# Kernel optimization log

Hardware: AMD Instinct MI355X
Metric: run time of the kernel (lower is better)

## Reference

```python
import jax, jax.numpy as jnp
import numpy as np

D = 200; H = 4; DH = D // H
N_ETYPE = 38; N_NTYPE = 4
B = 256; L = 1024; E = B * L
NODES_PER_G = 200; N = B * NODES_PER_G


def _bn(x, g, b):
    # BatchNorm1d in training mode: batch stats over rows (biased variance, eps=1e-5)
    m = x.mean(axis=0)
    v = x.var(axis=0)
    return (x - m) * jax.lax.rsqrt(v + 1e-5) * g + b


def setup_inputs():
    key = jax.random.key(0)
    ks = jax.random.split(key, 24)
    f = lambda k, s: jax.random.normal(k, s, jnp.float32) * 0.02
    head = jax.random.randint(ks[0], (E,), 0, N)
    tail = (head + 1 + jax.random.randint(ks[1], (E,), 0, N - 1)) % N  # guaranteed no self-loops
    return {
        "x": jax.random.normal(ks[2], (N, D), jnp.float32),
        "node_feature_extra": jax.random.normal(ks[3], (N, D), jnp.float32),
        "sent_vec_r": jax.random.normal(ks[4], (B, D), jnp.float32),
        "We1": f(ks[5], (N_ETYPE + 1 + 2 * N_NTYPE, D)), "be1": jnp.zeros((D,), jnp.float32),
        "ge1": jnp.ones((D,), jnp.float32), "bte1": jnp.zeros((D,), jnp.float32),
        "We2": f(ks[6], (D, D)), "be2": jnp.zeros((D,), jnp.float32),
        "Wa1": f(ks[7], (2 * D, D)), "ba1": jnp.zeros((D,), jnp.float32),
        "ga1": jnp.ones((D,), jnp.float32), "bta1": jnp.zeros((D,), jnp.float32),
        "Wa2": f(ks[8], (D, D)), "ba2": jnp.zeros((D,), jnp.float32),
        "Watt": f(ks[9], (D, D)),
        "Wk": f(ks[10], (2 * D, D)), "bk": jnp.zeros((D,), jnp.float32),
        "Wm": f(ks[11], (2 * D, D)), "bm": jnp.zeros((D,), jnp.float32),
        "Wq": f(ks[12], (D, D)), "bq": jnp.zeros((D,), jnp.float32),
        "Wo1": f(ks[13], (D, D)), "bo1": jnp.zeros((D,), jnp.float32),
        "go1": jnp.ones((D,), jnp.float32), "bto1": jnp.zeros((D,), jnp.float32),
        "Wo2": f(ks[14], (D, D)), "bo2": jnp.zeros((D,), jnp.float32),
        "edge_index": jnp.stack([head, tail]),
        "edge_type": jax.random.randint(ks[15], (E,), 0, N_ETYPE),
        "node_type": jax.random.randint(ks[16], (N,), 0, N_NTYPE),
        "edges_per_graph": L,
    }


def reference(x, node_feature_extra, sent_vec_r, We1, be1, ge1, bte1, We2, be2,
              Wa1, ba1, ga1, bta1, Wa2, ba2, Watt, Wk, bk, Wm, bm, Wq, bq,
              Wo1, bo1, go1, bto1, Wo2, bo2,
              edge_index, edge_type, node_type, edges_per_graph):
    E_, N_ = edge_index.shape[1], x.shape[0]
    src, dst = edge_index[0], edge_index[1]
    x_head, x_tail = x[src], x[dst]
    x_fact = x_tail - x_head
    nt = N_ETYPE + 1
    # original does this segment-mean on detached CPU numpy -> no gradient path
    xf = jax.lax.stop_gradient(x_fact)
    sums = jax.ops.segment_sum(xf, edge_type, num_segments=nt)
    cnts = jax.ops.segment_sum(jnp.ones((E_,), x.dtype), edge_type, num_segments=nt)
    result = (sums / jnp.maximum(cnts, 1.0)[:, None])[edge_type]  # [E, D]
    # one-hot edge/node-type features for real edges + self edges
    edge_vec = jax.nn.one_hot(edge_type, nt, dtype=x.dtype)
    self_edge_vec = jnp.zeros((N_, nt), x.dtype).at[:, N_ETYPE].set(1.0)
    ht = jnp.concatenate([jax.nn.one_hot(node_type[src], N_NTYPE, dtype=x.dtype),
                          jax.nn.one_hot(node_type[dst], N_NTYPE, dtype=x.dtype)], 1)
    sh = jax.nn.one_hot(node_type, N_NTYPE, dtype=x.dtype)
    feat = jnp.concatenate([jnp.concatenate([edge_vec, ht], 1),
                            jnp.concatenate([self_edge_vec, sh, sh], 1)], 0)  # [E+N, 47]
    emb = jax.nn.relu(_bn(feat @ We1 + be1, ge1, bte1)) @ We2 + be2  # edge_encoder, [E+N, D]
    emb_e, emb_self = emb[:E_], emb[E_:]
    # edge_encoder_again on cat([emb_e, result]); split matmul avoids the [E,2D] concat
    h2 = _bn(emb_e @ Wa1[:D] + result @ Wa1[D:] + ba1, ga1, bta1)
    R = jax.nn.relu(h2) @ Wa2 + ba2  # [E, D]
    # per-graph attention: Q rows within a graph are identical (repeated sent_vec),
    # so the LxL softmax has identical rows -> compute one row per graph and broadcast.
    Bg = E_ // edges_per_graph
    Rg = R.reshape(Bg, edges_per_graph, D)
    q = sent_vec_r @ Watt  # [B, D]
    scores = jnp.einsum('bd,bld->bl', q, Rg) / jnp.sqrt(jnp.asarray(D, x.dtype))
    attn = jax.nn.softmax(scores, axis=1)
    upd = jnp.einsum('bl,bld->bd', attn, Rg)
    updated_R = jnp.broadcast_to(upd[:, None, :], Rg.shape).reshape(E_, D)
    edge_attr = jnp.concatenate([updated_R, emb_self], 0)
    # append self-loops (input edge_index has none, matching remove_self_loops)
    loop = jnp.arange(N_, dtype=src.dtype)
    src_all = jnp.concatenate([src, loop])
    dst_all = jnp.concatenate([dst, loop])
    x_i, x_j = x[dst_all], x[src_all]
    key_ = (x_i @ Wk[:D] + edge_attr @ Wk[D:] + bk).reshape(-1, H, DH)
    msg = (x_j @ Wm[:D] + edge_attr @ Wm[D:] + bm).reshape(-1, H, DH)
    qry = ((x_j @ Wq + bq) / jnp.sqrt(jnp.asarray(DH, x.dtype))).reshape(-1, H, DH)
    sc = (qry * key_).sum(-1)  # [E+N, H]
    # segment softmax grouped by source node (every segment non-empty due to self-loops)
    smax = jax.ops.segment_max(sc, src_all, num_segments=N_)
    ex = jnp.exp(sc - smax[src_all])
    den = jax.ops.segment_sum(ex, src_all, num_segments=N_)
    alpha = ex / den[src_all]
    cnt = jax.ops.segment_sum(jnp.ones((src_all.shape[0],), x.dtype), src_all, num_segments=N_)
    alpha = alpha * cnt[src_all][:, None]
    m = (msg * alpha[:, :, None]).reshape(-1, D)
    aggr = jax.ops.segment_sum(m, dst_all, num_segments=N_)  # scatter-add at targets
    return jax.nn.relu(_bn(aggr @ Wo1 + bo1, go1, bto1)) @ Wo2 + bo2
```

## Files before the change

kernel.cpp:

```cpp
#include <hip/hip_runtime.h>

#define D     200
#define H     4
#define DH    50
#define NE    38
#define NTY   4
#define NC    608
#define NCT   612
#define BG    256
#define LG    1024
#define EE    262144
#define NN    51200
#define EA    313344
#define NB    200

#define NTILES 13
#define KSTEPS 7
#define NMATS  8
#define SLICE_SHORTS 13312
#define NCHUNK 26
#define MROWS  128

typedef __attribute__((ext_vector_type(4))) float  f32x4;
typedef __attribute__((ext_vector_type(8))) short  bf16x8;

__device__ __forceinline__ short bf_hi(float f) {
    unsigned u = __float_as_uint(f);
    unsigned r = u + 0x7fffu + ((u >> 16) & 1u);
    return (short)(r >> 16);
}
__device__ __forceinline__ float bf_f(short s) {
    return __uint_as_float(((unsigned)(unsigned short)s) << 16);
}

__global__ __launch_bounds__(256) void k_hist(const int* __restrict__ ei, const int* __restrict__ et,
                                              const int* __restrict__ nt, int* outdeg, int* indeg,
                                              int* __restrict__ hcnt, float* coef) {
    __shared__ int loc[NC];
    int g = blockIdx.x, t = threadIdx.x;
    for (int i = t; i < NC; i += 256) loc[i] = 0;
    __syncthreads();
    #pragma unroll
    for (int j = 0; j < 4; j++) {
        int e = g * LG + j * 256 + t;
        int s = ei[e], d = ei[EE + e], tp = et[e];
        int c = tp * 16 + nt[s] * 4 + nt[d];
        atomicAdd(&loc[c], 1);
        atomicAdd(&outdeg[s], 1);
        atomicAdd(&indeg[d], 1);
        unsafeAtomicAdd(&coef[(size_t)d * NE + tp],  1.f);
        unsafeAtomicAdd(&coef[(size_t)s * NE + tp], -1.f);
    }
    __syncthreads();
    for (int i = t; i < NC; i += 256) hcnt[g * NC + i] = loc[i];
}

__global__ __launch_bounds__(256) void k_hist2(const int* __restrict__ hcnt, int* __restrict__ hist) {
    int c = blockIdx.x * 256 + threadIdx.x;
    if (c >= NC) return;
    int s = 0;
    for (int g = 0; g < BG; g++) s += hcnt[g * NC + c];
    hist[c] = s;
}

__global__ __launch_bounds__(256) void k_ntcnt(const int* __restrict__ nt, int* ntcnt) {
    __shared__ int loc[NTY];
    int t = threadIdx.x;
    if (t < NTY) loc[t] = 0;
    __syncthreads();
    int n = blockIdx.x * 256 + t;
    if (n < NN) atomicAdd(&loc[nt[n]], 1);
    __syncthreads();
    if (t < NTY) atomicAdd(&ntcnt[t], loc[t]);
}

__global__ void k_tcnt(const int* __restrict__ hist, int* tcnt) {
    int t = threadIdx.x;
    if (t < NE) { int s = 0; for (int i = 0; i < 16; i++) s += hist[t*16 + i]; tcnt[t] = s; }
}

__global__ __launch_bounds__(256) void k_xfsum3(const float* __restrict__ x, const float* __restrict__ coef,
                                                float* sums) {
    const int CH = NN / 256;
    int t = threadIdx.x;
    int n0 = blockIdx.x * CH;
    float acc[NE];
    #pragma unroll
    for (int m = 0; m < NE; m++) acc[m] = 0.f;
    if (t < D) {
        for (int k = 0; k < CH; k++) {
            int n = n0 + k;
            float xv = x[(size_t)n * D + t];
            const float* cf = coef + (size_t)n * NE;
            #pragma unroll
            for (int m = 0; m < NE; m++) acc[m] += cf[m] * xv;
        }
        #pragma unroll
        for (int m = 0; m < NE; m++)
            if (acc[m] != 0.f) unsafeAtomicAdd(&sums[m * D + t], acc[m]);
    }
}

__global__ __launch_bounds__(256) void k_scan_a(const int* __restrict__ a, const int* __restrict__ b,
                                                int* bsA, int* bsB) {
    __shared__ int redA[4], redB[4];
    int t = threadIdx.x, blk = blockIdx.x;
    int i = blk * 256 + t;
    int va = a[i], vb = b[i];
    for (int o = 1; o < 64; o <<= 1) { va += __shfl_xor(va, o); vb += __shfl_xor(vb, o); }
    int wave = t >> 6, lane = t & 63;
    if (lane == 0) { redA[wave] = va; redB[wave] = vb; }
    __syncthreads();
    if (t == 0) {
        bsA[blk] = redA[0] + redA[1] + redA[2] + redA[3];
        bsB[blk] = redB[0] + redB[1] + redB[2] + redB[3];
    }
}

__global__ __launch_bounds__(256) void k_scan_b(int* bsA, int* bsB, int* aoff, int* boff) {
    __shared__ int pa[256], pb[256];
    int t = threadIdx.x;
    int va = (t < NB) ? bsA[t] : 0;
    int vb = (t < NB) ? bsB[t] : 0;
    pa[t] = va; pb[t] = vb;
    __syncthreads();
    for (int off = 1; off < 256; off <<= 1) {
        int xa = (t >= off) ? pa[t - off] : 0;
        int xb = (t >= off) ? pb[t - off] : 0;
        __syncthreads();
        pa[t] += xa; pb[t] += xb;
        __syncthreads();
    }
    if (t < NB) { bsA[t] = pa[t] - va; bsB[t] = pb[t] - vb; }
    if (t == NB - 1) { aoff[NN] = pa[t]; boff[NN] = pb[t]; }
}

__global__ __launch_bounds__(256) void k_scan_c(const int* __restrict__ a, const int* __restrict__ b,
                                                const int* __restrict__ bsA, const int* __restrict__ bsB,
                                                int* aoff, int* boff, int* acur, int* bcur) {
    __shared__ int wsA[4], wsB[4];
    int t = threadIdx.x, blk = blockIdx.x;
    int i = blk * 256 + t;
    int va = a[i], vb = b[i];
    int wave = t >> 6, lane = t & 63;
    int sa = va, sb = vb;
    for (int o = 1; o < 64; o <<= 1) {
        int xa = __shfl_up(sa, o);
        int xb = __shfl_up(sb, o);
        if (lane >= o) { sa += xa; sb += xb; }
    }
    if (lane == 63) { wsA[wave] = sa; wsB[wave] = sb; }
    __syncthreads();
    int baseA = bsA[blk], baseB = bsB[blk];
    #pragma unroll
    for (int wv = 0; wv < 3; wv++) {
        if (wv < wave) { baseA += wsA[wv]; baseB += wsB[wv]; }
    }
    int ea = baseA + sa - va;
    int eb = baseB + sb - vb;
    aoff[i] = ea; acur[i] = ea;
    boff[i] = eb; bcur[i] = eb;
}

__global__ __launch_bounds__(256) void k_scatter(const int* __restrict__ ei, int* scur, int* dcur,
                                                 int* slist, int* dlist) {
    int e = blockIdx.x * 256 + threadIdx.x;
    if (e >= EE) return;
    int s = ei[e], d = ei[EE + e];
    slist[atomicAdd(&scur[s], 1)] = e;
    dlist[atomicAdd(&dcur[d], 1)] = e;
}

__global__ __launch_bounds__(256) void k_combos1(const float* __restrict__ We1, const float* __restrict__ be1,
                                                 const int* __restrict__ hist, const int* __restrict__ ntcnt,
                                                 float* __restrict__ h1, float* bn1) {
    int c = blockIdx.x, d = threadIdx.x;
    if (d >= D) return;
    float v, w;
    if (c < NC) {
        int etp = c >> 4, ts = (c >> 2) & 3, td = c & 3;
        v = We1[etp*D + d] + We1[(39+ts)*D + d] + We1[(43+td)*D + d] + be1[d];
        w = (float)hist[c];
    } else {
        int t = c - NC;
        v = We1[38*D + d] + We1[(39+t)*D + d] + We1[(43+t)*D + d] + be1[d];
        w = (float)ntcnt[t];
    }
    h1[c*D + d] = v;
    unsafeAtomicAdd(&bn1[d], w * v);
    unsafeAtomicAdd(&bn1[D + d], w * v * v);
}

__global__ __launch_bounds__(256) void k_combos2(const float* __restrict__ h1, const float* __restrict__ bn1,
                                                 const float* __restrict__ ge1, const float* __restrict__ bte1,
                                                 const float* __restrict__ We2, const float* __restrict__ be2,
                                                 float* __restrict__ embE, float* __restrict__ embS) {
    __shared__ float v[D];
    int c = blockIdx.x, t = threadIdx.x;
    if (t < D) {
        float cnt = (float)(EE + NN);
        float m = bn1[t] / cnt;
        float var = bn1[D + t] / cnt - m * m;
        float r = rsqrtf(var + 1e-5f);
        float u = (h1[c*D + t] - m) * r * ge1[t] + bte1[t];
        v[t] = fmaxf(u, 0.f);
    }
    __syncthreads();
    if (t < D) {
        float acc = be2[t];
        for (int k = 0; k < D; k++) acc += v[k] * We2[k*D + t];
        if (c < NC) embE[c*D + t] = acc; else embS[(c-NC)*D + t] = acc;
    }
}

__global__ __launch_bounds__(256) void k_combos3(const float* __restrict__ embE, const float* __restrict__ sumsxf,
                                                 const int* __restrict__ tcnt, const float* __restrict__ Wa1,
                                                 const float* __restrict__ ba1, const int* __restrict__ hist,
                                                 float* __restrict__ h2, float* bn2) {
    __shared__ float a[2*D];
    int c = blockIdx.x, t = threadIdx.x;
    int etp = c >> 4;
    if (t < D) {
        a[t] = embE[c*D + t];
        float cn = fmaxf((float)tcnt[etp], 1.f);
        a[D + t] = sumsxf[etp*D + t] / cn;
    }
    __syncthreads();
    if (t < D) {
        float acc = ba1[t];
        for (int k = 0; k < 2*D; k++) acc += a[k] * Wa1[k*D + t];
        h2[c*D + t] = acc;
        float w = (float)hist[c];
        unsafeAtomicAdd(&bn2[t], w * acc);
        unsafeAtomicAdd(&bn2[D + t], w * acc * acc);
    }
}

__global__ __launch_bounds__(256) void k_combos4(const float* __restrict__ h2, const float* __restrict__ bn2,
                                                 const float* __restrict__ ga1, const float* __restrict__ bta1,
                                                 const float* __restrict__ Wa2, const float* __restrict__ ba2,
                                                 float* __restrict__ Rc, float* __restrict__ RcT) {
    __shared__ float v[D];
    int c = blockIdx.x, t = threadIdx.x;
    if (t < D) {
        float inv = 1.f / (float)EE;
        float m = bn2[t] * inv;
        float var = bn2[D + t] * inv - m * m;
        float r = rsqrtf(var + 1e-5f);
        float u = (h2[c*D + t] - m) * r * ga1[t] + bta1[t];
        v[t] = fmaxf(u, 0.f);
    }
    __syncthreads();
    if (t < D) {
        float acc = ba2[t];
        for (int k = 0; k < D; k++) acc += v[k] * Wa2[k*D + t];
        Rc[c*D + t] = acc;
        RcT[(size_t)t * NC + c] = acc;
    }
}

__global__ __launch_bounds__(512) void k_attn(const float* __restrict__ qs,
                                              const float* __restrict__ Rc, const float* __restrict__ RcT,
                                              const int* __restrict__ hcnt, float* __restrict__ upd) {
    __shared__ float q[D];
    __shared__ float w[NC];
    __shared__ float red[16];
    __shared__ float part[8][D];
    int b = blockIdx.x, t = threadIdx.x;
    int wave = t >> 6, lane = t & 63;
    if (t < D) q[t] = qs[b*D + t];
    __syncthreads();
    {
        float s0a = 0.f, s0b = 0.f, s0c = 0.f, s0d = 0.f;
        float s1a = 0.f, s1b = 0.f, s1c = 0.f, s1d = 0.f;
        for (int k = 0; k < D; k += 4) {
            float q0 = q[k], q1 = q[k+1], q2 = q[k+2], q3 = q[k+3];
            const float* r = RcT + (size_t)k * NC;
            s0a += q0 * r[t];
            s0b += q1 * r[NC + t];
            s0c += q2 * r[2*NC + t];
            s0d += q3 * r[3*NC + t];
            if (t < NC - 512) {
                s1a += q0 * r[t + 512];
                s1b += q1 * r[NC + t + 512];
                s1c += q2 * r[2*NC + t + 512];
                s1d += q3 * r[3*NC + t + 512];
            }
        }
        w[t] = (s0a + s0b) + (s0c + s0d);
        if (t < NC - 512) w[t + 512] = (s1a + s1b) + (s1c + s1d);
    }
    __syncthreads();
    float mx = -1e30f;
    for (int c = t; c < NC; c += 512) mx = fmaxf(mx, w[c]);
    for (int o = 32; o; o >>= 1) mx = fmaxf(mx, __shfl_xor(mx, o));
    if (lane == 0) red[wave] = mx;
    __syncthreads();
    mx = red[0];
    #pragma unroll
    for (int i = 1; i < 8; i++) mx = fmaxf(mx, red[i]);
    float sm = 0.f;
    for (int c = t; c < NC; c += 512) {
        float wv = (float)hcnt[b * NC + c] * __expf(w[c] - mx);
        w[c] = wv;
        sm += wv;
    }
    for (int o = 32; o; o >>= 1) sm += __shfl_xor(sm, o);
    if (lane == 0) red[8 + wave] = sm;
    __syncthreads();
    float tot = red[8];
    #pragma unroll
    for (int i = 1; i < 8; i++) tot += red[8 + i];
    float inv = 1.f / tot;
    float a4[4] = {0.f, 0.f, 0.f, 0.f};
    for (int c = wave * (NC/8); c < (wave + 1) * (NC/8); c++) {
        float wv = w[c];
        const float* r = Rc + c * D;
        #pragma unroll
        for (int j = 0; j < 4; j++) { int dd = lane + 64*j; if (dd < D) a4[j] += wv * r[dd]; }
    }
    #pragma unroll
    for (int j = 0; j < 4; j++) { int dd = lane + 64*j; if (dd < D) part[wave][dd] = a4[j]; }
    __syncthreads();
    if (t < D) {
        float s = part[0][t];
        #pragma unroll
        for (int i = 1; i < 8; i++) s += part[i][t];
        upd[b*D + t] = s * inv;
    }
}

__global__ __launch_bounds__(256) void k_packW(const float* __restrict__ Wk, const float* __restrict__ Wm,
                                               const float* __restrict__ Wq, const float* __restrict__ Wo1,
                                               const float* __restrict__ Wo2, const float* __restrict__ Watt,
                                               short* __restrict__ Bpk) {
    int blk = blockIdx.x;
    int mat = blk / (NTILES * KSTEPS);
    int rem = blk - mat * (NTILES * KSTEPS);
    int ks = rem / NTILES, nt = rem - ks * NTILES;
    const float* W = (mat == 0) ? Wk : (mat == 1) ? Wm : (mat == 2) ? Wq : (mat == 3) ? Wo1 :
                     (mat == 4) ? Wo2 : (mat == 5) ? Watt : (mat == 6) ? (Wk + D*D) : (Wm + D*D);
    int t = threadIdx.x;
    for (int idx = t; idx < 1024; idx += 256) {
        int split = idx >> 9;
        int lane = (idx & 511) >> 3;
        int j = idx & 7;
        int n = nt * 16 + (lane & 15);
        int k = ks * 32 + ((lane >> 4) << 3) + j;
        float v = (k < D && n < D) ? W[k * D + n] : 0.f;
        short h = bf_hi(v);
        short out = split ? bf_hi(v - bf_f(h)) : h;
        Bpk[(size_t)blk * 1024 + idx] = out;
    }
}

__device__ __forceinline__ void stage_load(const short* __restrict__ g, int w, int lane, f32x4 rg[7]) {
    #pragma unroll
    for (int i = 0; i < 7; i++) {
        int c = w + 4 * i;
        if (c < NCHUNK) rg[i] = *(const f32x4*)((const char*)g + c * 1024 + lane * 16);
    }
}
__device__ __forceinline__ void stage_write(short* l, int w, int lane, const f32x4 rg[7]) {
    #pragma unroll
    for (int i = 0; i < 7; i++) {
        int c = w + 4 * i;
        if (c < NCHUNK) *(f32x4*)((char*)l + c * 1024 + lane * 16) = rg[i];
    }
}

__device__ __forceinline__ void load_afrag(const float* __restrict__ A, int row, int quad, int ks,
                                           int preop, const float* __restrict__ bnacc, float invCnt,
                                           const float* __restrict__ g, const float* __restrict__ bb,
                                           bf16x8& ah, bf16x8& al) {
    int k0 = ks * 32 + quad * 8;
    float v[8];
    if (k0 < D) {
        const float* src = A + (size_t)row * D + k0;
        float4 p0 = *(const float4*)src;
        float4 p1 = *(const float4*)(src + 4);
        v[0]=p0.x; v[1]=p0.y; v[2]=p0.z; v[3]=p0.w;
        v[4]=p1.x; v[5]=p1.y; v[6]=p1.z; v[7]=p1.w;
        if (preop) {
            float4 m0 = *(const float4*)(bnacc + k0);
            float4 m1 = *(const float4*)(bnacc + k0 + 4);
            float4 q0 = *(const float4*)(bnacc + D + k0);
            float4 q1 = *(const float4*)(bnacc + D + k0 + 4);
            float4 g0 = *(const float4*)(g + k0);
            float4 g1 = *(const float4*)(g + k0 + 4);
            float4 b0 = *(const float4*)(bb + k0);
            float4 b1 = *(const float4*)(bb + k0 + 4);
            float mm[8] = {m0.x,m0.y,m0.z,m0.w,m1.x,m1.y,m1.z,m1.w};
            float qq[8] = {q0.x,q0.y,q0.z,q0.w,q1.x,q1.y,q1.z,q1.w};
            float gg[8] = {g0.x,g0.y,g0.z,g0.w,g1.x,g1.y,g1.z,g1.w};
            float bv[8] = {b0.x,b0.y,b0.z,b0.w,b1.x,b1.y,b1.z,b1.w};
            #pragma unroll
            for (int j = 0; j < 8; j++) {
                float mj = mm[j] * invCnt;
                float var = qq[j] * invCnt - mj * mj;
                float rs = rsqrtf(var + 1e-5f);
                float s = rs * gg[j];
                v[j] = fmaxf(v[j] * s + (bv[j] - mj * s), 0.f);
            }
        }
    } else {
        #pragma unroll
        for (int j = 0; j < 8; j++) v[j] = 0.f;
    }
    #pragma unroll
    for (int j = 0; j < 8; j++) {
        short h = bf_hi(v[j]);
        ah[j] = h;
        al[j] = bf_hi(v[j] - bf_f(h));
    }
}

__device__ __forceinline__ void store_C2(f32x4 acc0[NTILES], f32x4 acc1[NTILES], float* __restrict__ C,
                                         int n0, int w, int lane,
                                         const float* __restrict__ bias, float postscale) {
    int colb = lane & 15, quad = lane >> 4;
    int rbase = n0 + w * 32;
    #pragma unroll
    for (int nt = 0; nt < NTILES; nt++) {
        int col = nt * 16 + colb;
        if (col < D) {
            float bj = bias ? bias[col] : 0.f;
            #pragma unroll
            for (int r = 0; r < 4; r++) {
                int row = rbase + quad * 4 + r;
                C[(size_t)row * D + col]        = (acc0[nt][r] + bj) * postscale;
                C[(size_t)(row + 16) * D + col] = (acc1[nt][r] + bj) * postscale;
            }
        }
    }
}

#define MMF_KS(MATV, KS, NUTOT, BASE)                                           \
    {                                                                           \
        int u_ = (MATV) * KSTEPS + (KS);                                        \
        int cur_ = u_ & 1;                                                      \
        if (u_ + 1 < (NUTOT))                                                   \
            stage_load((BASE) + (size_t)(u_ + 1) * SLICE_SHORTS, w, lane, rg);  \
        bf16x8 ah0_, al0_, ah1_, al1_;                                          \
        load_afrag(A, row0, quad, KS, preop_, bnacc_, invCnt_, g_, bb_, ah0_, al0_); \
        load_afrag(A, row1, quad, KS, preop_, bnacc_, invCnt_, g_, bb_, ah1_, al1_); \
        const bf16x8* B8_ = (const bf16x8*)(Bls + cur_ * SLICE_SHORTS);         \
        _Pragma("unroll")                                                       \
        for (int nt = 0; nt < NTILES; nt++) {                                   \
            bf16x8 bh = B8_[nt * 128 + lane];                                   \
            bf16x8 bl = B8_[nt * 128 + 64 + lane];                              \
            acc0[nt] = __builtin_amdgcn_mfma_f32_16x16x32_bf16(al0_, bh, acc0[nt], 0, 0, 0); \
            acc0[nt] = __builtin_amdgcn_mfma_f32_16x16x32_bf16(ah0_, bl, acc0[nt], 0, 0, 0); \
            acc0[nt] = __builtin_amdgcn_mfma_f32_16x16x32_bf16(ah0_, bh, acc0[nt], 0, 0, 0); \
            acc1[nt] = __builtin_amdgcn_mfma_f32_16x16x32_bf16(al1_, bh, acc1[nt], 0, 0, 0); \
            acc1[nt] = __builtin_amdgcn_mfma_f32_16x16x32_bf16(ah1_, bl, acc1[nt], 0, 0, 0); \
            acc1[nt] = __builtin_amdgcn_mfma_f32_16x16x32_bf16(ah1_, bh, acc1[nt], 0, 0, 0); \
        }                                                                       \
        if (u_ + 1 < (NUTOT)) {                                                 \
            stage_write(Bls + (cur_ ^ 1) * SLICE_SHORTS, w, lane, rg);          \
            __syncthreads();                                                    \
        }                                                                       \
    }

__global__ __launch_bounds__(256, 2) void k_mmf3(const float* __restrict__ A, const short* __restrict__ Bpk,
                                                 const float* __restrict__ bq,
                                                 float* __restrict__ XK, float* __restrict__ XM, float* __restrict__ XQ) {
    __shared__ __align__(16) short Bls[2 * SLICE_SHORTS];
    int t = threadIdx.x, w = t >> 6, lane = t & 63;
    int n0 = blockIdx.x * MROWS;
    int row0 = n0 + w * 32 + (lane & 15);
    int row1 = row0 + 16;
    int quad = lane >> 4;
    int preop_ = 0; const float* bnacc_ = nullptr; float invCnt_ = 0.f;
    const float* g_ = nullptr; const float* bb_ = nullptr;
    f32x4 rg[7];
    stage_load(Bpk, w, lane, rg);
    stage_write(Bls, w, lane, rg);
    __syncthreads();
    f32x4 acc0[NTILES], acc1[NTILES];
    for (int mat = 0; mat < 3; ++mat) {
        #pragma unroll
        for (int nt = 0; nt < NTILES; nt++) {
            acc0[nt][0]=0.f; acc0[nt][1]=0.f; acc0[nt][2]=0.f; acc0[nt][3]=0.f;
            acc1[nt][0]=0.f; acc1[nt][1]=0.f; acc1[nt][2]=0.f; acc1[nt][3]=0.f;
        }
        MMF_KS(mat, 0, 3*KSTEPS, Bpk)
        MMF_KS(mat, 1, 3*KSTEPS, Bpk)
        MMF_KS(mat, 2, 3*KSTEPS, Bpk)
        MMF_KS(mat, 3, 3*KSTEPS, Bpk)
        MMF_KS(mat, 4, 3*KSTEPS, Bpk)
        MMF_KS(mat, 5, 3*KSTEPS, Bpk)
        MMF_KS(mat, 6, 3*KSTEPS, Bpk)
        if (mat == 0)      store_C2(acc0, acc1, XK, n0, w, lane, nullptr, 1.f);
        else if (mat == 1) store_C2(acc0, acc1, XM, n0, w, lane, nullptr, 1.f);
        else               store_C2(acc0, acc1, XQ, n0, w, lane, bq, 0.14142135623730950488f);
    }
}

__global__ __launch_bounds__(256, 2) void k_mmf(const float* __restrict__ A, const short* __restrict__ Bmat,
                                                const float* __restrict__ bias, float* __restrict__ C,
                                                int preop, const float* __restrict__ bnacc, float invCnt,
                                                const float* __restrict__ g, const float* __restrict__ bb,
                                                float postscale) {
    __shared__ __align__(16) short Bls[2 * SLICE_SHORTS];
    int t = threadIdx.x, w = t >> 6, lane = t & 63;
    int n0 = blockIdx.x * MROWS;
    int row0 = n0 + w * 32 + (lane & 15);
    int row1 = row0 + 16;
    int quad = lane >> 4;
    int preop_ = preop; const float* bnacc_ = bnacc; float invCnt_ = invCnt;
    const float* g_ = g; const float* bb_ = bb;
    f32x4 rg[7];
    stage_load(Bmat, w, lane, rg);
    stage_write(Bls, w, lane, rg);
    __syncthreads();
    f32x4 acc0[NTILES], acc1[NTILES];
    #pragma unroll
    for (int nt = 0; nt < NTILES; nt++) {
        acc0[nt][0]=0.f; acc0[nt][1]=0.f; acc0[nt][2]=0.f; acc0[nt][3]=0.f;
        acc1[nt][0]=0.f; acc1[nt][1]=0.f; acc1[nt][2]=0.f; acc1[nt][3]=0.f;
    }
    MMF_KS(0, 0, KSTEPS, Bmat)
    MMF_KS(0, 1, KSTEPS, Bmat)
    MMF_KS(0, 2, KSTEPS, Bmat)
    MMF_KS(0, 3, KSTEPS, Bmat)
    MMF_KS(0, 4, KSTEPS, Bmat)
    MMF_KS(0, 5, KSTEPS, Bmat)
    MMF_KS(0, 6, KSTEPS, Bmat)
    store_C2(acc0, acc1, C, n0, w, lane, bias, postscale);
}

__device__ __forceinline__ float head_reduce(float h0, float h1, float h2, float h3, int lane) {
    float ax = (lane < 32) ? h2 : h0;
    float ay = (lane < 32) ? h3 : h1;
    float u0 = ((lane < 32) ? h0 : h2) + __shfl_xor(ax, 32);
    float u1 = ((lane < 32) ? h1 : h3) + __shfl_xor(ay, 32);
    float bx = ((lane & 16) == 0) ? u1 : u0;
    float v  = (((lane & 16) == 0) ? u0 : u1) + __shfl_xor(bx, 16);
    v += __shfl_xor(v, 8);
    v += __shfl_xor(v, 4);
    v += __shfl_xor(v, 2);
    v += __shfl_xor(v, 1);
    return v;
}

__global__ __launch_bounds__(256) void k_soft(const int* __restrict__ ei, const int* __restrict__ nt,
                                              const int* __restrict__ soff, const int* __restrict__ slist,
                                              const int* __restrict__ outdeg,
                                              const float* __restrict__ XQ, const float* __restrict__ XK,
                                              const float* __restrict__ GK, const float* __restrict__ SK,
                                              float* __restrict__ sc, float* __restrict__ scale) {
    int wave = threadIdx.x >> 6, lane = threadIdx.x & 63;
    int n = blockIdx.x * 4 + wave;
    if (n >= NN) return;
    bool act = lane < DH;
    int grp = lane >> 4;
    float qv0 = 0.f, qv1 = 0.f, qv2 = 0.f, qv3 = 0.f;
    if (act) {
        const float* q = XQ + (size_t)n * D + lane;
        qv0 = q[0]; qv1 = q[DH]; qv2 = q[2*DH]; qv3 = q[3*DH];
    }
    float den = 0.f;
    {
        int tn = nt[n];
        float h0 = 0.f, h1 = 0.f, h2 = 0.f, h3 = 0.f;
        if (act) {
            const float* xk = XK + (size_t)n * D + lane;
            const float* sk = SK + (size_t)tn * D + lane;
            h0 = qv0 * (xk[0]    + sk[0]);
            h1 = qv1 * (xk[DH]   + sk[DH]);
            h2 = qv2 * (xk[2*DH] + sk[2*DH]);
            h3 = qv3 * (xk[3*DH] + sk[3*DH]);
        }
        float v = head_reduce(h0, h1, h2, h3, lane);
        float e = __expf(v);
        den += e;
        if ((lane & 15) == 0) sc[(size_t)(EE + n) * 4 + grp] = e;
    }
    int beg = soff[n], end = soff[n + 1];
    for (int i = beg; i < end; i++) {
        int e_ = slist[i];
        int tail = ei[EE + e_];
        int g = e_ >> 10;
        float h0 = 0.f, h1 = 0.f, h2 = 0.f, h3 = 0.f;
        if (act) {
            const float* xk = XK + (size_t)tail * D + lane;
            const float* gk = GK + (size_t)g * D + lane;
            h0 = qv0 * (xk[0]    + gk[0]);
            h1 = qv1 * (xk[DH]   + gk[DH]);
            h2 = qv2 * (xk[2*DH] + gk[2*DH]);
            h3 = qv3 * (xk[3*DH] + gk[3*DH]);
        }
        float v = head_reduce(h0, h1, h2, h3, lane);
        float e = __expf(v);
        den += e;
        if ((lane & 15) == 0) sc[(size_t)e_ * 4 + grp] = e;
    }
    float cnt = (float)(outdeg[n] + 1);
    if ((lane & 15) == 0) scale[(size_t)n * 4 + grp] = cnt / den;
}

__global__ __launch_bounds__(256) void k_aggr(const int* __restrict__ ei, const int* __restrict__ nt,
                                              const int* __restrict__ doff, const int* __restrict__ dlist,
                                              const float* __restrict__ sc, const float* __restrict__ scale,
                                              const float* __restrict__ XM, const float* __restrict__ GM,
                                              const float* __restrict__ SM, float* __restrict__ aggr) {
    int wave = threadIdx.x >> 6, lane = threadIdx.x & 63;
    int n = blockIdx.x * 4 + wave;
    if (n >= NN) return;
    bool act = lane < DH;
    float acc0 = 0.f, acc1 = 0.f, acc2 = 0.f, acc3 = 0.f;
    {
        int tn = nt[n];
        float4 ss = *(const float4*)&sc[(size_t)(EE + n) * 4];
        float4 sl = *(const float4*)&scale[(size_t)n * 4];
        if (act) {
            const float* xm = XM + (size_t)n * D + lane;
            const float* sm = SM + (size_t)tn * D + lane;
            acc0 += ss.x * sl.x * (xm[0]    + sm[0]);
            acc1 += ss.y * sl.y * (xm[DH]   + sm[DH]);
            acc2 += ss.z * sl.z * (xm[2*DH] + sm[2*DH]);
            acc3 += ss.w * sl.w * (xm[3*DH] + sm[3*DH]);
        }
    }
    int beg = doff[n], end = doff[n + 1];
    for (int i = beg; i < end; i++) {
        int e = dlist[i];
        int s = ei[e];
        int g = e >> 10;
        float4 ss = *(const float4*)&sc[(size_t)e * 4];
        float4 sl = *(const float4*)&scale[(size_t)s * 4];
        if (act) {
            const float* xm = XM + (size_t)s * D + lane;
            const float* gm = GM + (size_t)g * D + lane;
            acc0 += ss.x * sl.x * (xm[0]    + gm[0]);
            acc1 += ss.y * sl.y * (xm[DH]   + gm[DH]);
            acc2 += ss.z * sl.z * (xm[2*DH] + gm[2*DH]);
            acc3 += ss.w * sl.w * (xm[3*DH] + gm[3*DH]);
        }
    }
    if (act) {
        float* out = aggr + (size_t)n * D + lane;
        out[0]    = acc0;
        out[DH]   = acc1;
        out[2*DH] = acc2;
        out[3*DH] = acc3;
    }
}

__global__ __launch_bounds__(256) void k_colstats(const float* __restrict__ T1, float* bn3) {
    int t = threadIdx.x;
    if (t >= D) return;
    int r0 = blockIdx.x * 256;
    float s = 0.f, q = 0.f;
    for (int r = r0; r < r0 + 256; r++) {
        float v = T1[(size_t)r * D + t];
        s += v; q += v * v;
    }
    unsafeAtomicAdd(&bn3[t], s);
    unsafeAtomicAdd(&bn3[D + t], q);
}

extern "C" void kernel_launch(void* const* d_in, const int* in_sizes, int n_in,
                              void* d_out, int out_size, void* d_ws, size_t ws_size,
                              hipStream_t stream) {
    const float* x    = (const float*)d_in[0];
    const float* sent = (const float*)d_in[2];
    const float* We1  = (const float*)d_in[3];
    const float* be1  = (const float*)d_in[4];
    const float* ge1  = (const float*)d_in[5];
    const float* bte1 = (const float*)d_in[6];
    const float* We2  = (const float*)d_in[7];
    const float* be2  = (const float*)d_in[8];
    const float* Wa1  = (const float*)d_in[9];
    const float* ba1  = (const float*)d_in[10];
    const float* ga1  = (const float*)d_in[11];
    const float* bta1 = (const float*)d_in[12];
    const float* Wa2  = (const float*)d_in[13];
    const float* ba2  = (const float*)d_in[14];
    const float* Watt = (const float*)d_in[15];
    const float* Wk   = (const float*)d_in[16];
    const float* bk   = (const float*)d_in[17];
    const float* Wm   = (const float*)d_in[18];
    const float* bm   = (const float*)d_in[19];
    const float* Wq   = (const float*)d_in[20];
    const float* bq   = (const float*)d_in[21];
    const float* Wo1  = (const float*)d_in[22];
    const float* bo1  = (const float*)d_in[23];
    const float* go1  = (const float*)d_in[24];
    const float* bto1 = (const float*)d_in[25];
    const float* Wo2  = (const float*)d_in[26];
    const float* bo2  = (const float*)d_in[27];
    const int* ei = (const int*)d_in[28];
    const int* et = (const int*)d_in[29];
    const int* nt = (const int*)d_in[30];

    char* ws = (char*)d_ws;
    size_t off = 0;
    auto alloc = [&](size_t bytes) -> char* {
        char* p = ws + off;
        off = (off + bytes + 255) & ~(size_t)255;
        return p;
    };
    int*   hist   = (int*)  alloc(NC * 4);
    int*   ntcnt  = (int*)  alloc(NTY * 4);
    float* bn1    = (float*)alloc(2 * D * 4);
    float* bn2    = (float*)alloc(2 * D * 4);
    float* bn3    = (float*)alloc(2 * D * 4);
    float* sumsxf = (float*)alloc(NE * D * 4);
    int*   outdeg = (int*)  alloc(NN * 4);
    int*   indeg  = (int*)  alloc(NN * 4);
    int*   hcnt   = (int*)  alloc((size_t)BG * NC * 4);
    float* updS   = (float*)alloc((size_t)384 * D * 4);
    size_t zero_end = off;
    int* tcnt = (int*)alloc(NE * 4);
    int* soff_ = (int*)alloc((NN + 1) * 4);
    int* doff_ = (int*)alloc((NN + 1) * 4);
    int* scur = (int*)alloc(NN * 4);
    int* dcur = (int*)alloc(NN * 4);
    int* bsA  = (int*)alloc(NB * 4);
    int* bsB  = (int*)alloc(NB * 4);
    int* slist = (int*)alloc((size_t)EE * 4);
    int* dlist = (int*)alloc((size_t)EE * 4);
    short* Bpk  = (short*)alloc((size_t)NMATS * NTILES * KSTEPS * 1024 * 2);
    float* h1v   = (float*)alloc((size_t)NCT * D * 4);
    float* embE  = (float*)alloc((size_t)NC * D * 4);
    float* h2pre = (float*)alloc((size_t)NC * D * 4);
    float* Rc    = (float*)alloc((size_t)NC * D * 4);
    float* RcT   = (float*)alloc((size_t)D * NC * 4);
    float* qs    = (float*)alloc((size_t)BG * D * 4);
    float* GK    = (float*)alloc((size_t)384 * D * 4);
    float* GM    = (float*)alloc((size_t)384 * D * 4);
    float* sc    = (float*)alloc((size_t)EA * H * 4);
    float* XK    = (float*)alloc((size_t)NN * D * 4);
    float* XM    = (float*)alloc((size_t)NN * D * 4);
    float* XQ    = (float*)alloc((size_t)NN * D * 4);
    float* coef  = XK;
    float* scale = h1v;
    float* aggr  = XQ;
    float* T1    = XK;
    float* embS  = updS + 256 * D;
    float* SK    = GK + 256 * D;
    float* SM    = GM + 256 * D;

    const int matstride = NTILES * KSTEPS * 1024;

    hipMemsetAsync(ws, 0, zero_end, stream);
    hipMemsetAsync(coef, 0, (size_t)NN * NE * 4, stream);

    k_packW  <<<NMATS * NTILES * KSTEPS, 256, 0, stream>>>(Wk, Wm, Wq, Wo1, Wo2, Watt, Bpk);
    k_hist   <<<BG, 256, 0, stream>>>(ei, et, nt, outdeg, indeg, hcnt, coef);
    k_hist2  <<<3, 256, 0, stream>>>(hcnt, hist);
    k_ntcnt  <<<NN / 256, 256, 0, stream>>>(nt, ntcnt);
    k_tcnt   <<<1, 64, 0, stream>>>(hist, tcnt);
    k_scan_a <<<NB, 256, 0, stream>>>(outdeg, indeg, bsA, bsB);
    k_scan_b <<<1, 256, 0, stream>>>(bsA, bsB, soff_, doff_);
    k_scan_c <<<NB, 256, 0, stream>>>(outdeg, indeg, bsA, bsB, soff_, doff_, scur, dcur);
    k_scatter<<<EE / 256, 256, 0, stream>>>(ei, scur, dcur, slist, dlist);
    k_xfsum3 <<<256, 256, 0, stream>>>(x, coef, sumsxf);
    k_mmf    <<<BG / MROWS, 256, 0, stream>>>(sent, Bpk + (size_t)5 * matstride, nullptr, qs,
                                              0, nullptr, 0.f, nullptr, nullptr, 0.07071067811865475f);
    k_combos1<<<NCT, 256, 0, stream>>>(We1, be1, hist, ntcnt, h1v, bn1);
    k_combos2<<<NCT, 256, 0, stream>>>(h1v, bn1, ge1, bte1, We2, be2, embE, embS);
    k_combos3<<<NC, 256, 0, stream>>>(embE, sumsxf, tcnt, Wa1, ba1, hist, h2pre, bn2);
    k_combos4<<<NC, 256, 0, stream>>>(h2pre, bn2, ga1, bta1, Wa2, ba2, Rc, RcT);
    k_attn   <<<BG, 512, 0, stream>>>(qs, Rc, RcT, hcnt, updS);
    k_mmf    <<<3, 256, 0, stream>>>(updS, Bpk + (size_t)6 * matstride, bk, GK,
                                     0, nullptr, 0.f, nullptr, nullptr, 1.f);
    k_mmf    <<<3, 256, 0, stream>>>(updS, Bpk + (size_t)7 * matstride, bm, GM,
                                     0, nullptr, 0.f, nullptr, nullptr, 1.f);
    k_mmf3   <<<NN / MROWS, 256, 0, stream>>>(x, Bpk, bq, XK, XM, XQ);
    k_soft   <<<NN / 4, 256, 0, stream>>>(ei, nt, soff_, slist, outdeg, XQ, XK, GK, SK, sc, scale);
    k_aggr   <<<NN / 4, 256, 0, stream>>>(ei, nt, doff_, dlist, sc, scale, XM, GM, SM, aggr);
    k_mmf    <<<NN / MROWS, 256, 0, stream>>>(aggr, Bpk + (size_t)3 * matstride, bo1, T1,
                                              0, nullptr, 0.f, nullptr, nullptr, 1.f);
    k_colstats<<<NN / 256, 256, 0, stream>>>(T1, bn3);
    k_mmf    <<<NN / MROWS, 256, 0, stream>>>(T1, Bpk + (size_t)4 * matstride, bo2, (float*)d_out,
                                              1, bn3, 1.f / (float)NN, go1, bto1, 1.f);
}
```

Baseline: 1.010 ms.

## Split GEMM column tiles across two waves per row group with 512-thread blocks

The MFMA GEMM kernels now use 8 waves per block instead of 4. Each pair of waves shares one 32-row group and splits the 13 column tiles 7/6, so each wave holds about half as many accumulators. Staging of the B slice is spread over 8 waves. This cuts per-wave register pressure and raises waves in flight to hide latency. In exchange, the A-fragment loads and bf16 split are duplicated across the two waves of each pair, and 512-thread blocks may lower the number of blocks resident per CU.

```diff
diff --git a/kernel.cpp b/kernel.cpp
--- a/kernel.cpp
+++ b/kernel.cpp
@@ -354,17 +354,17 @@
     }
 }
 
-__device__ __forceinline__ void stage_load(const short* __restrict__ g, int w, int lane, f32x4 rg[7]) {
-    #pragma unroll
-    for (int i = 0; i < 7; i++) {
-        int c = w + 4 * i;
+__device__ __forceinline__ void stage_load8(const short* __restrict__ g, int w, int lane, f32x4 rg[4]) {
+    #pragma unroll
+    for (int i = 0; i < 4; i++) {
+        int c = w + 8 * i;
         if (c < NCHUNK) rg[i] = *(const f32x4*)((const char*)g + c * 1024 + lane * 16);
     }
 }
-__device__ __forceinline__ void stage_write(short* l, int w, int lane, const f32x4 rg[7]) {
-    #pragma unroll
-    for (int i = 0; i < 7; i++) {
-        int c = w + 4 * i;
+__device__ __forceinline__ void stage_write8(short* l, int w, int lane, const f32x4 rg[4]) {
+    #pragma unroll
+    for (int i = 0; i < 4; i++) {
+        int c = w + 8 * i;
         if (c < NCHUNK) *(f32x4*)((char*)l + c * 1024 + lane * 16) = rg[i];
     }
 }
@@ -415,21 +415,23 @@
     }
 }
 
-__device__ __forceinline__ void store_C2(f32x4 acc0[NTILES], f32x4 acc1[NTILES], float* __restrict__ C,
-                                         int n0, int w, int lane,
+__device__ __forceinline__ void store_C2(f32x4 acc0[7], f32x4 acc1[7], float* __restrict__ C,
+                                         int n0, int rowg, int ntb, int ntn, int lane,
                                          const float* __restrict__ bias, float postscale) {
     int colb = lane & 15, quad = lane >> 4;
-    int rbase = n0 + w * 32;
-    #pragma unroll
-    for (int nt = 0; nt < NTILES; nt++) {
-        int col = nt * 16 + colb;
-        if (col < D) {
-            float bj = bias ? bias[col] : 0.f;
-            #pragma unroll
-            for (int r = 0; r < 4; r++) {
-                int row = rbase + quad * 4 + r;
-                C[(size_t)row * D + col]        = (acc0[nt][r] + bj) * postscale;
-                C[(size_t)(row + 16) * D + col] = (acc1[nt][r] + bj) * postscale;
+    int rbase = n0 + rowg * 32 + quad * 4;
+    #pragma unroll
+    for (int nt = 0; nt < 7; nt++) {
+        if (nt < ntn) {
+            int col = (ntb + nt) * 16 + colb;
+            if (col < D) {
+                float bj = bias ? bias[col] : 0.f;
+                #pragma unroll
+                for (int r = 0; r < 4; r++) {
+                    int row = rbase + r;
+                    C[(size_t)row * D + col]        = (acc0[nt][r] + bj) * postscale;
+                    C[(size_t)(row + 16) * D + col] = (acc1[nt][r] + bj) * postscale;
+                }
             }
         }
     }
@@ -440,47 +442,51 @@
         int u_ = (MATV) * KSTEPS + (KS);                                        \
         int cur_ = u_ & 1;                                                      \
         if (u_ + 1 < (NUTOT))                                                   \
-            stage_load((BASE) + (size_t)(u_ + 1) * SLICE_SHORTS, w, lane, rg);  \
+            stage_load8((BASE) + (size_t)(u_ + 1) * SLICE_SHORTS, w, lane, rg); \
         bf16x8 ah0_, al0_, ah1_, al1_;                                          \
         load_afrag(A, row0, quad, KS, preop_, bnacc_, invCnt_, g_, bb_, ah0_, al0_); \
         load_afrag(A, row1, quad, KS, preop_, bnacc_, invCnt_, g_, bb_, ah1_, al1_); \
         const bf16x8* B8_ = (const bf16x8*)(Bls + cur_ * SLICE_SHORTS);         \
         _Pragma("unroll")                                                       \
-        for (int nt = 0; nt < NTILES; nt++) {                                   \
-            bf16x8 bh = B8_[nt * 128 + lane];                                   \
-            bf16x8 bl = B8_[nt * 128 + 64 + lane];                              \
-            acc0[nt] = __builtin_amdgcn_mfma_f32_16x16x32_bf16(al0_, bh, acc0[nt], 0, 0, 0); \
-            acc0[nt] = __builtin_amdgcn_mfma_f32_16x16x32_bf16(ah0_, bl, acc0[nt], 0, 0, 0); \
-            acc0[nt] = __builtin_amdgcn_mfma_f32_16x16x32_bf16(ah0_, bh, acc0[nt], 0, 0, 0); \
-            acc1[nt] = __builtin_amdgcn_mfma_f32_16x16x32_bf16(al1_, bh, acc1[nt], 0, 0, 0); \
-            acc1[nt] = __builtin_amdgcn_mfma_f32_16x16x32_bf16(ah1_, bl, acc1[nt], 0, 0, 0); \
-            acc1[nt] = __builtin_amdgcn_mfma_f32_16x16x32_bf16(ah1_, bh, acc1[nt], 0, 0, 0); \
+        for (int nt = 0; nt < 7; nt++) {                                        \
+            if (nt < ntn) {                                                     \
+                bf16x8 bh = B8_[(ntb + nt) * 128 + lane];                       \
+                bf16x8 bl = B8_[(ntb + nt) * 128 + 64 + lane];                  \
+                acc0[nt] = __builtin_amdgcn_mfma_f32_16x16x32_bf16(al0_, bh, acc0[nt], 0, 0, 0); \
+                acc0[nt] = __builtin_amdgcn_mfma_f32_16x16x32_bf16(ah0_, bl, acc0[nt], 0, 0, 0); \
+                acc0[nt] = __builtin_amdgcn_mfma_f32_16x16x32_bf16(ah0_, bh, acc0[nt], 0, 0, 0); \
+                acc1[nt] = __builtin_amdgcn_mfma_f32_16x16x32_bf16(al1_, bh, acc1[nt], 0, 0, 0); \
+                acc1[nt] = __builtin_amdgcn_mfma_f32_16x16x32_bf16(ah1_, bl, acc1[nt], 0, 0, 0); \
+                acc1[nt] = __builtin_amdgcn_mfma_f32_16x16x32_bf16(ah1_, bh, acc1[nt], 0, 0, 0); \
+            }                                                                   \
         }                                                                       \
         if (u_ + 1 < (NUTOT)) {                                                 \
-            stage_write(Bls + (cur_ ^ 1) * SLICE_SHORTS, w, lane, rg);          \
+            stage_write8(Bls + (cur_ ^ 1) * SLICE_SHORTS, w, lane, rg);         \
             __syncthreads();                                                    \
         }                                                                       \
     }
 
-__global__ __launch_bounds__(256, 2) void k_mmf3(const float* __restrict__ A, const short* __restrict__ Bpk,
+__global__ __launch_bounds__(512, 2) void k_mmf3(const float* __restrict__ A, const short* __restrict__ Bpk,
                                                  const float* __restrict__ bq,
                                                  float* __restrict__ XK, float* __restrict__ XM, float* __restrict__ XQ) {
     __shared__ __align__(16) short Bls[2 * SLICE_SHORTS];
     int t = threadIdx.x, w = t >> 6, lane = t & 63;
     int n0 = blockIdx.x * MROWS;
-    int row0 = n0 + w * 32 + (lane & 15);
+    int rowg = w >> 1, colg = w & 1;
+    int ntb = colg * 7, ntn = colg ? 6 : 7;
+    int row0 = n0 + rowg * 32 + (lane & 15);
     int row1 = row0 + 16;
     int quad = lane >> 4;
     int preop_ = 0; const float* bnacc_ = nullptr; float invCnt_ = 0.f;
     const float* g_ = nullptr; const float* bb_ = nullptr;
-    f32x4 rg[7];
-    stage_load(Bpk, w, lane, rg);
-    stage_write(Bls, w, lane, rg);
-    __syncthreads();
-    f32x4 acc0[NTILES], acc1[NTILES];
+    f32x4 rg[4];
+    stage_load8(Bpk, w, lane, rg);
+    stage_write8(Bls, w, lane, rg);
+    __syncthreads();
+    f32x4 acc0[7], acc1[7];
     for (int mat = 0; mat < 3; ++mat) {
         #pragma unroll
-        for (int nt = 0; nt < NTILES; nt++) {
+        for (int nt = 0; nt < 7; nt++) {
             acc0[nt][0]=0.f; acc0[nt][1]=0.f; acc0[nt][2]=0.f; acc0[nt][3]=0.f;
             acc1[nt][0]=0.f; acc1[nt][1]=0.f; acc1[nt][2]=0.f; acc1[nt][3]=0.f;
         }
@@ -491,13 +497,13 @@
         MMF_KS(mat, 4, 3*KSTEPS, Bpk)
         MMF_KS(mat, 5, 3*KSTEPS, Bpk)
         MMF_KS(mat, 6, 3*KSTEPS, Bpk)
-        if (mat == 0)      store_C2(acc0, acc1, XK, n0, w, lane, nullptr, 1.f);
-        else if (mat == 1) store_C2(acc0, acc1, XM, n0, w, lane, nullptr, 1.f);
-        else               store_C2(acc0, acc1, XQ, n0, w, lane, bq, 0.14142135623730950488f);
-    }
-}
-
-__global__ __launch_bounds__(256, 2) void k_mmf(const float* __restrict__ A, const short* __restrict__ Bmat,
+        if (mat == 0)      store_C2(acc0, acc1, XK, n0, rowg, ntb, ntn, lane, nullptr, 1.f);
+        else if (mat == 1) store_C2(acc0, acc1, XM, n0, rowg, ntb, ntn, lane, nullptr, 1.f);
+        else               store_C2(acc0, acc1, XQ, n0, rowg, ntb, ntn, lane, bq, 0.14142135623730950488f);
+    }
+}
+
+__global__ __launch_bounds__(512, 2) void k_mmf(const float* __restrict__ A, const short* __restrict__ Bmat,
                                                 const float* __restrict__ bias, float* __restrict__ C,
                                                 int preop, const float* __restrict__ bnacc, float invCnt,
                                                 const float* __restrict__ g, const float* __restrict__ bb,
@@ -505,18 +511,20 @@
     __shared__ __align__(16) short Bls[2 * SLICE_SHORTS];
     int t = threadIdx.x, w = t >> 6, lane = t & 63;
     int n0 = blockIdx.x * MROWS;
-    int row0 = n0 + w * 32 + (lane & 15);
+    int rowg = w >> 1, colg = w & 1;
+    int ntb = colg * 7, ntn = colg ? 6 : 7;
+    int row0 = n0 + rowg * 32 + (lane & 15);
     int row1 = row0 + 16;
     int quad = lane >> 4;
     int preop_ = preop; const float* bnacc_ = bnacc; float invCnt_ = invCnt;
     const float* g_ = g; const float* bb_ = bb;
-    f32x4 rg[7];
-    stage_load(Bmat, w, lane, rg);
-    stage_write(Bls, w, lane, rg);
-    __syncthreads();
-    f32x4 acc0[NTILES], acc1[NTILES];
-    #pragma unroll
-    for (int nt = 0; nt < NTILES; nt++) {
+    f32x4 rg[4];
+    stage_load8(Bmat, w, lane, rg);
+    stage_write8(Bls, w, lane, rg);
+    __syncthreads();
+    f32x4 acc0[7], acc1[7];
+    #pragma unroll
+    for (int nt = 0; nt < 7; nt++) {
         acc0[nt][0]=0.f; acc0[nt][1]=0.f; acc0[nt][2]=0.f; acc0[nt][3]=0.f;
         acc1[nt][0]=0.f; acc1[nt][1]=0.f; acc1[nt][2]=0.f; acc1[nt][3]=0.f;
     }
@@ -527,7 +535,7 @@
     MMF_KS(0, 4, KSTEPS, Bmat)
     MMF_KS(0, 5, KSTEPS, Bmat)
     MMF_KS(0, 6, KSTEPS, Bmat)
-    store_C2(acc0, acc1, C, n0, w, lane, bias, postscale);
+    store_C2(acc0, acc1, C, n0, rowg, ntb, ntn, lane, bias, postscale);
 }
 
 __device__ __forceinline__ float head_reduce(float h0, float h1, float h2, float h3, int lane) {
@@ -758,23 +766,23 @@
     k_scan_c <<<NB, 256, 0, stream>>>(outdeg, indeg, bsA, bsB, soff_, doff_, scur, dcur);
     k_scatter<<<EE / 256, 256, 0, stream>>>(ei, scur, dcur, slist, dlist);
     k_xfsum3 <<<256, 256, 0, stream>>>(x, coef, sumsxf);
-    k_mmf    <<<BG / MROWS, 256, 0, stream>>>(sent, Bpk + (size_t)5 * matstride, nullptr, qs,
+    k_mmf    <<<BG / MROWS, 512, 0, stream>>>(sent, Bpk + (size_t)5 * matstride, nullptr, qs,
                                               0, nullptr, 0.f, nullptr, nullptr, 0.07071067811865475f);
     k_combos1<<<NCT, 256, 0, stream>>>(We1, be1, hist, ntcnt, h1v, bn1);
     k_combos2<<<NCT, 256, 0, stream>>>(h1v, bn1, ge1, bte1, We2, be2, embE, embS);
     k_combos3<<<NC, 256, 0, stream>>>(embE, sumsxf, tcnt, Wa1, ba1, hist, h2pre, bn2);
     k_combos4<<<NC, 256, 0, stream>>>(h2pre, bn2, ga1, bta1, Wa2, ba2, Rc, RcT);
     k_attn   <<<BG, 512, 0, stream>>>(qs, Rc, RcT, hcnt, updS);
-    k_mmf    <<<3, 256, 0, stream>>>(updS, Bpk + (size_t)6 * matstride, bk, GK,
+    k_mmf    <<<3, 512, 0, stream>>>(updS, Bpk + (size_t)6 * matstride, bk, GK,
                                      0, nullptr, 0.f, nullptr, nullptr, 1.f);
-    k_mmf    <<<3, 256, 0, stream>>>(updS, Bpk + (size_t)7 * matstride, bm, GM,
+    k_mmf    <<<3, 512, 0, stream>>>(updS, Bpk + (size_t)7 * matstride, bm, GM,
                                      0, nullptr, 0.f, nullptr, nullptr, 1.f);
-    k_mmf3   <<<NN / MROWS, 256, 0, stream>>>(x, Bpk, bq, XK, XM, XQ);
+    k_mmf3   <<<NN / MROWS, 512, 0, stream>>>(x, Bpk, bq, XK, XM, XQ);
     k_soft   <<<NN / 4, 256, 0, stream>>>(ei, nt, soff_, slist, outdeg, XQ, XK, GK, SK, sc, scale);
     k_aggr   <<<NN / 4, 256, 0, stream>>>(ei, nt, doff_, dlist, sc, scale, XM, GM, SM, aggr);
-    k_mmf    <<<NN / MROWS, 256, 0, stream>>>(aggr, Bpk + (size_t)3 * matstride, bo1, T1,
+    k_mmf    <<<NN / MROWS, 512, 0, stream>>>(aggr, Bpk + (size_t)3 * matstride, bo1, T1,
                                               0, nullptr, 0.f, nullptr, nullptr, 1.f);
     k_colstats<<<NN / 256, 256, 0, stream>>>(T1, bn3);
-    k_mmf    <<<NN / MROWS, 256, 0, stream>>>(T1, Bpk + (size_t)4 * matstride, bo2, (float*)d_out,
+    k_mmf    <<<NN / MROWS, 512, 0, stream>>>(T1, Bpk + (size_t)4 * matstride, bo2, (float*)d_out,
                                               1, bn3, 1.f / (float)NN, go1, bto1, 1.f);
 }
```

New measurement: 886.6 us. 12.2% less time.
